# Performance work log

Hardware: AMD Instinct MI355X
Metric: run time of the kernel (lower is better)

## Reference

```python
import jax, jax.numpy as jnp
import numpy as np

L, H, F, FH, MLPD = 12, 12, 768, 64, 3072  # layers, heads, d_model, head_dim, mlp hidden
GH, GW = 32, 32
N = 1 + GH * GW  # cls token + patches
EPS = 1e-6
QK_SCALE = FH ** (-0.5)
STAGE_ENDS = (2, 5, 8, 11)  # last layer index of each of the 4 stages (3 layers/stage)


def _relpos_index(h, w):
    # standard timm BEiT relative position index with 3 extra cls entries
    coords = np.stack(np.meshgrid(np.arange(h), np.arange(w), indexing="ij"))  # 2,h,w
    cf = coords.reshape(2, -1)
    rel = (cf[:, :, None] - cf[:, None, :]).transpose(1, 2, 0).astype(np.int64)  # hw,hw,2
    rel[:, :, 0] += h - 1
    rel[:, :, 1] += w - 1
    rel[:, :, 0] *= 2 * w - 1
    num_rel = (2 * h - 1) * (2 * w - 1) + 3
    idx = np.zeros((h * w + 1, h * w + 1), dtype=np.int32)
    idx[1:, 1:] = rel.sum(-1)
    idx[0, 0:] = num_rel - 3
    idx[0:, 0] = num_rel - 2
    idx[0, 0] = num_rel - 1
    return idx, num_rel


def setup_inputs() -> dict:
    key = jax.random.key(0)
    ks = jax.random.split(key, 10)
    s = 0.02
    idx, R = _relpos_index(GH, GW)
    return dict(
        patch_tokens=jax.random.normal(ks[0], (1, GH * GW, F), jnp.float32),
        cls_token=jax.random.normal(ks[1], (1, 1, F), jnp.float32) * s,
        ln1_w=jnp.ones((L, F), jnp.float32),
        ln1_b=jnp.zeros((L, F), jnp.float32),
        qkv_w=jax.random.normal(ks[2], (L, 3 * F, F), jnp.float32) * s,
        q_bias=jax.random.normal(ks[3], (L, H, FH), jnp.float32) * s,
        v_bias=jax.random.normal(ks[4], (L, H, FH), jnp.float32) * s,
        proj_w=jax.random.normal(ks[5], (L, F, F), jnp.float32) * s,
        proj_b=jnp.zeros((L, F), jnp.float32),
        scale_attn=jnp.full((L, F), 0.1, jnp.float32),
        ln2_w=jnp.ones((L, F), jnp.float32),
        ln2_b=jnp.zeros((L, F), jnp.float32),
        fc1_w=jax.random.normal(ks[6], (L, MLPD, F), jnp.float32) * s,
        fc1_b=jnp.zeros((L, MLPD), jnp.float32),
        fc2_w=jax.random.normal(ks[7], (L, F, MLPD), jnp.float32) * s,
        fc2_b=jnp.zeros((L, F), jnp.float32),
        scale_mlp=jnp.full((L, F), 0.1, jnp.float32),
        relpos_table=jax.random.normal(ks[8], (L, R, H), jnp.float32) * s,
        relpos_index=jnp.asarray(idx),
        patch_grid_hw=jnp.array([GH, GW], jnp.int32),
    )


def _ln(x, w, b):
    mu = jnp.mean(x, -1, keepdims=True)
    var = jnp.mean(jnp.square(x - mu), -1, keepdims=True)
    return (x - mu) * jax.lax.rsqrt(var + EPS) * w + b


def reference(patch_tokens, cls_token, ln1_w, ln1_b, qkv_w, q_bias, v_bias,
              proj_w, proj_b, scale_attn, ln2_w, ln2_b, fc1_w, fc1_b, fc2_w,
              fc2_b, scale_mlp, relpos_table, relpos_index, patch_grid_hw):
    B = patch_tokens.shape[0]
    tokens = jnp.concatenate(
        [jnp.broadcast_to(cls_token, (B, 1, F)), patch_tokens], axis=1)  # B,N,F

    params = dict(ln1_w=ln1_w, ln1_b=ln1_b, qkv_w=qkv_w, q_bias=q_bias,
                  v_bias=v_bias, proj_w=proj_w, proj_b=proj_b,
                  scale_attn=scale_attn, ln2_w=ln2_w, ln2_b=ln2_b,
                  fc1_w=fc1_w, fc1_b=fc1_b, fc2_w=fc2_w, fc2_b=fc2_b,
                  scale_mlp=scale_mlp, relpos_table=relpos_table)

    def step(x, p):
        h = _ln(x, p['ln1_w'], p['ln1_b'])
        qkv = jnp.einsum('bnf,gf->bng', h, p['qkv_w'])          # B,N,3F (no bias)
        qkv = qkv.reshape(B, N, 3, H, FH).transpose(2, 0, 3, 1, 4)
        q, k, v = qkv[0], qkv[1], qkv[2]                         # B,H,N,fh
        q = (q + p['q_bias'][None, :, None, :]) * QK_SCALE
        v = v + p['v_bias'][None, :, None, :]
        bias = p['relpos_table'][relpos_index]                   # N,N,H
        attn = jnp.einsum('bhnd,bhmd->bhnm', q, k) + bias.transpose(2, 0, 1)[None]
        w = jax.nn.softmax(attn, axis=-1)
        o = jnp.einsum('bhnm,bhmd->bhnd', w, v).transpose(0, 2, 1, 3).reshape(B, N, F)
        o = o @ p['proj_w'].T + p['proj_b']
        x = x + p['scale_attn'] * o
        h2 = _ln(x, p['ln2_w'], p['ln2_b'])
        m = jax.nn.gelu(h2 @ p['fc1_w'].T + p['fc1_b'], approximate=False)
        m = m @ p['fc2_w'].T + p['fc2_b']
        x = x + p['scale_mlp'] * m
        return x, x

    _, ys = jax.lax.scan(step, tokens, params)  # ys: L,B,N,F
    return (ys[STAGE_ENDS[0]], ys[STAGE_ENDS[1]], ys[STAGE_ENDS[2]], ys[STAGE_ENDS[3]])
```

## Files before the change

### kernel.cpp

```cpp
#include <hip/hip_runtime.h>
#include <hip/hip_bf16.h>
#include <math.h>

#define L_LAYERS 12
#define H_HEADS  12
#define F_DIM    768
#define FH_DIM   64
#define MLPD     3072
#define NT       1025
#define NTP      1056
#define THREE_F  2304
#define R_REL    3972
#define QK_SCALE 0.125f
#define QB       64
#define KB       128

#define CQKV  (THREE_F * F_DIM)
#define CPROJ (F_DIM * F_DIM)
#define CFC1  (MLPD * F_DIM)
#define CFC2  (F_DIM * MLPD)

typedef short short8_t __attribute__((ext_vector_type(8)));
typedef float f32x4_t  __attribute__((ext_vector_type(4)));
typedef __attribute__((address_space(1))) const void* gptr_t;
typedef __attribute__((address_space(3))) void*       lptr_t;

typedef __hip_bfloat16 bf16;

static __device__ inline unsigned short f2bf(float f) {
    __hip_bfloat16 b(f);
    unsigned short u;
    __builtin_memcpy(&u, &b, 2);
    return u;
}

__device__ inline void xcd_remap(int& tx, int& ty) {
    int gx = gridDim.x, gy = gridDim.y;
    int b = blockIdx.y * gx + blockIdx.x;
    int total = gx * gy;
    int q = total >> 3, r = total & 7;
    int xcd = b & 7, i = b >> 3;
    int pos = (xcd < r) ? xcd * (q + 1) + i : r * (q + 1) + (xcd - r) * q + i;
    ty = pos / gx;
    tx = pos - ty * gx;
}

__global__ void init_x_k(const float* __restrict__ patch, const float* __restrict__ cls,
                         float* __restrict__ x) {
    int i = blockIdx.x * 256 + threadIdx.x;
    if (i >= NT * F_DIM) return;
    int n = i / F_DIM, f = i - n * F_DIM;
    x[i] = (n == 0) ? cls[f] : patch[(size_t)(n - 1) * F_DIM + f];
}

__global__ void zero_vt_k(bf16* __restrict__ vt) {
    int i = blockIdx.x * 256 + threadIdx.x;
    int total = H_HEADS * FH_DIM * NTP;
    #pragma unroll
    for (int j = 0; j < 8; ++j) {
        int e = i * 8 + j;
        if (e < total) vt[e] = __hip_bfloat16(0.0f);
    }
}

__global__ void rp16_k(const int* __restrict__ rp, unsigned short* __restrict__ rp16) {
    int i = blockIdx.x * 256 + threadIdx.x;
    if (i < NT * NT) rp16[i] = (unsigned short)rp[i];
}

__global__ void tableT_k(const float* __restrict__ t, float* __restrict__ tt) {
    int i = blockIdx.x * 256 + threadIdx.x;
    if (i >= L_LAYERS * R_REL * H_HEADS) return;
    int l = i / (R_REL * H_HEADS), rem = i - l * (R_REL * H_HEADS);
    int rr = rem / H_HEADS, hh = rem - rr * H_HEADS;
    tt[((size_t)l * H_HEADS + hh) * R_REL + rr] = t[i];
}

__global__ void conv_all_k(const float* __restrict__ qkv_w, const float* __restrict__ proj_w,
                           const float* __restrict__ fc1_w, const float* __restrict__ fc2_w,
                           bf16* __restrict__ wq, bf16* __restrict__ wp,
                           bf16* __restrict__ w1, bf16* __restrict__ w2) {
    const long A1 = (long)L_LAYERS * CQKV;
    const long A2 = A1 + (long)L_LAYERS * CPROJ;
    const long A3 = A2 + (long)L_LAYERS * CFC1;
    const long A4 = A3 + (long)L_LAYERS * CFC2;
    const long total4 = A4 >> 2;
    for (long qd = (long)blockIdx.x * 256 + threadIdx.x; qd < total4;
         qd += (long)gridDim.x * 256) {
        long e = qd << 2;
        const float* s; bf16* d; long off;
        if (e < A1)      { s = qkv_w;  d = wq; off = e; }
        else if (e < A2) { s = proj_w; d = wp; off = e - A1; }
        else if (e < A3) { s = fc1_w;  d = w1; off = e - A2; }
        else             { s = fc2_w;  d = w2; off = e - A3; }
        float4 v = *reinterpret_cast<const float4*>(s + off);
        ushort4 o;
        o.x = f2bf(v.x); o.y = f2bf(v.y); o.z = f2bf(v.z); o.w = f2bf(v.w);
        *reinterpret_cast<ushort4*>(d + off) = o;
    }
}

__global__ void layernorm_k(const float* __restrict__ x, const float* __restrict__ w,
                            const float* __restrict__ b, bf16* __restrict__ out) {
    const int row = blockIdx.x;
    const float* xr = x + (size_t)row * F_DIM;
    float v0 = xr[threadIdx.x];
    float v1 = xr[threadIdx.x + 256];
    float v2 = xr[threadIdx.x + 512];
    float s  = v0 + v1 + v2;
    float s2 = v0 * v0 + v1 * v1 + v2 * v2;
    #pragma unroll
    for (int off = 32; off; off >>= 1) {
        s  += __shfl_down(s, off);
        s2 += __shfl_down(s2, off);
    }
    __shared__ float ws_[4], ws2_[4];
    int lane = threadIdx.x & 63, wid = threadIdx.x >> 6;
    if (lane == 0) { ws_[wid] = s; ws2_[wid] = s2; }
    __syncthreads();
    float S  = ws_[0] + ws_[1] + ws_[2] + ws_[3];
    float S2 = ws2_[0] + ws2_[1] + ws2_[2] + ws2_[3];
    float mu  = S * (1.0f / F_DIM);
    float var = S2 * (1.0f / F_DIM) - mu * mu;
    float rs  = rsqrtf(var + 1e-6f);
    bf16* orow = out + (size_t)row * F_DIM;
    orow[threadIdx.x]       = __hip_bfloat16((v0 - mu) * rs * w[threadIdx.x]       + b[threadIdx.x]);
    orow[threadIdx.x + 256] = __hip_bfloat16((v1 - mu) * rs * w[threadIdx.x + 256] + b[threadIdx.x + 256]);
    orow[threadIdx.x + 512] = __hip_bfloat16((v2 - mu) * rs * w[threadIdx.x + 512] + b[threadIdx.x + 512]);
}


template <int T, int NLOAD>
__device__ inline void stage_glds(const bf16* __restrict__ g0, int ld, int rows_rem,
                                  bf16* lds, int tid) {
    #pragma unroll
    for (int i = 0; i < NLOAD; ++i) {
        int slot = i * T + tid;
        int row = slot >> 3, s = slot & 7;
        int grow = row < rows_rem ? row : (rows_rem - 1);
        const bf16* src = g0 + (size_t)grow * ld + ((s ^ (row & 7)) * 8);
        bf16* dst = lds + (size_t)(i * T + (tid & ~63)) * 8;
        __builtin_amdgcn_global_load_lds((gptr_t)src, (lptr_t)dst, 16, 0, 0);
    }
}

template <int EPI, int BM, int BN, int WM, int WN>
__global__ __launch_bounds__((BM / (WM * 16)) * (BN / (WN * 16)) * 64)
void gemm_k(const bf16* __restrict__ A, const bf16* __restrict__ B,
            int M, int Nc, int K, int lda, int ldb,
            const float* __restrict__ p0, const float* __restrict__ p1,
            float* __restrict__ outF, float* __restrict__ outDup,
            bf16* __restrict__ outB0, bf16* __restrict__ outB1, bf16* __restrict__ outB2) {
    constexpr int NWM = BM / (WM * 16);
    constexpr int NWN = BN / (WN * 16);
    constexpr int T   = NWM * NWN * 64;
    constexpr int ALOADS = BM * 8 / T;
    constexpr int BLOADS = BN * 8 / T;

    __shared__ __align__(16) bf16 As[2][BM * 64];
    __shared__ __align__(16) bf16 Bs[2][BN * 64];

    int tx, ty;
    xcd_remap(tx, ty);
    const int tid  = threadIdx.x;
    const int lane = tid & 63, wid = tid >> 6;
    const int wr = wid / NWN, wc = wid % NWN;
    const int g4 = lane >> 4, l16 = lane & 15;
    const int bm = tx * BM, bn = ty * BN;
    const bf16* Ab = A + (size_t)bm * lda;
    const bf16* Bb = B + (size_t)bn * ldb;
    const int aRows = min(BM, M - bm);
    const int bRows = min(BN, Nc - bn);

    f32x4_t acc[WM][WN] = {};
    const int NK = K >> 6;

    stage_glds<T, ALOADS>(Ab, lda, aRows, As[0], tid);
    stage_glds<T, BLOADS>(Bb, ldb, bRows, Bs[0], tid);
    __syncthreads();

    for (int t = 0; t < NK; ++t) {
        const int c = t & 1;
        if (t + 1 < NK) {
            stage_glds<T, ALOADS>(Ab + (t + 1) * 64, lda, aRows, As[c ^ 1], tid);
            stage_glds<T, BLOADS>(Bb + (t + 1) * 64, ldb, bRows, Bs[c ^ 1], tid);
        }
        const short* AsS = reinterpret_cast<const short*>(As[c]);
        const short* BsS = reinterpret_cast<const short*>(Bs[c]);
        #pragma unroll
        for (int kk = 0; kk < 2; ++kk) {
            short8_t af[WM], bfr[WN];
            #pragma unroll
            for (int mi = 0; mi < WM; ++mi) {
                int ar = wr * WM * 16 + mi * 16 + l16;
                int j = (kk * 4 + g4) ^ (ar & 7);
                af[mi] = *reinterpret_cast<const short8_t*>(AsS + ar * 64 + j * 8);
            }
            #pragma unroll
            for (int ni = 0; ni < WN; ++ni) {
                int br = wc * WN * 16 + ni * 16 + l16;
                int j = (kk * 4 + g4) ^ (br & 7);
                bfr[ni] = *reinterpret_cast<const short8_t*>(BsS + br * 64 + j * 8);
            }
            #pragma unroll
            for (int mi = 0; mi < WM; ++mi)
                #pragma unroll
                for (int ni = 0; ni < WN; ++ni)
                    acc[mi][ni] = __builtin_amdgcn_mfma_f32_16x16x32_bf16(
                        af[mi], bfr[ni], acc[mi][ni], 0, 0, 0);
        }
        __syncthreads();
    }

    #pragma unroll
    for (int mi = 0; mi < WM; ++mi) {
        #pragma unroll
        for (int r = 0; r < 4; ++r) {
            const int row = bm + wr * WM * 16 + mi * 16 + g4 * 4 + r;
            if (row >= M) continue;
            #pragma unroll
            for (int ni = 0; ni < WN; ++ni) {
                const int col = bn + wc * WN * 16 + ni * 16 + l16;
                float v = acc[mi][ni][r];
                if (EPI == 0) {
                    if (col < F_DIM) {
                        int h = col >> 6, d = col & 63;
                        float q = (v + p0[col]) * QK_SCALE;
                        outB0[((size_t)h * NT + row) * 64 + d] = __hip_bfloat16(q);
                    } else if (col < 2 * F_DIM) {
                        int g = col - F_DIM;
                        int h = g >> 6, d = g & 63;
                        outB1[((size_t)h * NT + row) * 64 + d] = __hip_bfloat16(v);
                    } else {
                        int g = col - 2 * F_DIM;
                        int h = g >> 6, d = g & 63;
                        float vv = v + p1[g];
                        outB2[((size_t)h * 64 + d) * NTP + row] = __hip_bfloat16(vv);
                    }
                } else if (EPI == 3) {
                    size_t oi = (size_t)row * Nc + col;
                    v += p0[col];
                    float nv = outF[oi] + p1[col] * v;
                    outF[oi] = nv;
                    if (outDup) outDup[oi] = nv;
                } else if (EPI == 4) {
                    v += p0[col];
                    float g = 0.5f * v * (1.0f + erff(v * 0.70710678118654752f));
                    outB0[(size_t)row * MLPD + col] = __hip_bfloat16(g);
                }
            }
        }
    }
}

__global__ __launch_bounds__(256)
void flash_k(const bf16* __restrict__ q_bf, const bf16* __restrict__ k_bf,
             const bf16* __restrict__ v_t, const unsigned short* __restrict__ rp16,
             const float* __restrict__ tableT, bf16* __restrict__ o_bf) {
    __shared__ __align__(16) bf16 Qs[QB * 64];
    __shared__ __align__(16) bf16 Ks[2][KB * 64];
    __shared__ __align__(16) bf16 Vs[2][64 * KB];
    __shared__ __align__(16) bf16 Ps[4][16 * KB];

    int qx, h;
    xcd_remap(qx, h);
    const int tid = threadIdx.x, lane = tid & 63, w = tid >> 6;
    const int qb = qx * QB;
    const bf16* qh = q_bf + (size_t)h * NT * 64;
    const bf16* kh = k_bf + (size_t)h * NT * 64;
    const bf16* vh = v_t  + (size_t)h * 64 * NTP;
    const float* tbl = tableT + (size_t)h * R_REL;
    const int q_local = lane & 15;
    const int g4 = lane >> 4;

    auto stageKV = [&](int buf, int m0) {
        const int kRows = min(KB, NT - m0);
        #pragma unroll
        for (int i = 0; i < 4; ++i) {
            int slot = i * 256 + tid;
            int row = slot >> 3, s = slot & 7;
            int grow = min(row, kRows - 1);
            const bf16* src = kh + (size_t)(m0 + grow) * 64 + (s ^ (row & 7)) * 8;
            bf16* dst = Ks[buf] + (size_t)(i * 256 + (tid & ~63)) * 8;
            __builtin_amdgcn_global_load_lds((gptr_t)src, (lptr_t)dst, 16, 0, 0);
        }
        #pragma unroll
        for (int i = 0; i < 4; ++i) {
            int slot = i * 256 + tid;
            int d = slot >> 4, s = slot & 15;
            int msl = min(m0 / 8 + (s ^ (d & 15)), NTP / 8 - 1);
            const bf16* src = vh + (size_t)d * NTP + msl * 8;
            bf16* dst = Vs[buf] + (size_t)(i * 256 + (tid & ~63)) * 8;
            __builtin_amdgcn_global_load_lds((gptr_t)src, (lptr_t)dst, 16, 0, 0);
        }
    };

    {
        const int qRows = min(QB, NT - qb);
        #pragma unroll
        for (int i = 0; i < 2; ++i) {
            int slot = i * 256 + tid;
            int row = slot >> 3, s = slot & 7;
            int grow = min(row, qRows - 1);
            const bf16* src = qh + (size_t)(qb + grow) * 64 + (s ^ (row & 7)) * 8;
            bf16* dst = Qs + (size_t)(i * 256 + (tid & ~63)) * 8;
            __builtin_amdgcn_global_load_lds((gptr_t)src, (lptr_t)dst, 16, 0, 0);
        }
    }
    stageKV(0, 0);
    __syncthreads();

    short8_t qf[2];
    {
        const short* QsS = (const short*)Qs;
        #pragma unroll
        for (int kk = 0; kk < 2; ++kk) {
            int row = w * 16 + q_local;
            int slot = (kk * 4 + g4) ^ (row & 7);
            qf[kk] = *(const short8_t*)(QsS + row * 64 + slot * 8);
        }
    }

    float m_run[4], l_run[4];
    f32x4_t acc[4] = {};
    #pragma unroll
    for (int r = 0; r < 4; ++r) { m_run[r] = -1e30f; l_run[r] = 0.0f; }

    const int NTILES = (NT + KB - 1) / KB;
    for (int t = 0; t < NTILES; ++t) {
        const int m0 = t * KB;
        const int c = t & 1;
        if (t + 1 < NTILES) stageKV(c ^ 1, (t + 1) * KB);

        f32x4_t sfr[8];
        {
            const short* KsS = (const short*)Ks[c];
            #pragma unroll
            for (int f = 0; f < 8; ++f) {
                f32x4_t cacc = {};
                #pragma unroll
                for (int kk = 0; kk < 2; ++kk) {
                    int mrow = f * 16 + q_local;
                    int slot = (kk * 4 + g4) ^ (mrow & 7);
                    short8_t bv = *(const short8_t*)(KsS + mrow * 64 + slot * 8);
                    cacc = __builtin_amdgcn_mfma_f32_16x16x32_bf16(qf[kk], bv, cacc, 0, 0, 0);
                }
                sfr[f] = cacc;
            }
        }

        const int qrow_base = qb + w * 16 + g4 * 4;
        #pragma unroll
        for (int f = 0; f < 8; ++f) {
            int mm = m0 + f * 16 + q_local;
            if (mm < NT) {
                #pragma unroll
                for (int r = 0; r < 4; ++r) {
                    int qc = min(qrow_base + r, NT - 1);
                    int idx = rp16[(size_t)qc * NT + mm];
                    sfr[f][r] += tbl[idx];
                }
            } else {
                #pragma unroll
                for (int r = 0; r < 4; ++r) sfr[f][r] = -1e30f;
            }
        }

        float pmax[4];
        #pragma unroll
        for (int r = 0; r < 4; ++r) {
            float mx = sfr[0][r];
            #pragma unroll
            for (int f = 1; f < 8; ++f) mx = fmaxf(mx, sfr[f][r]);
            pmax[r] = mx;
        }
        #pragma unroll
        for (int off = 1; off < 16; off <<= 1)
            #pragma unroll
            for (int r = 0; r < 4; ++r) pmax[r] = fmaxf(pmax[r], __shfl_xor(pmax[r], off));

        float fac[4];
        #pragma unroll
        for (int r = 0; r < 4; ++r) {
            float mnew = fmaxf(m_run[r], pmax[r]);
            fac[r] = __expf(m_run[r] - mnew);
            m_run[r] = mnew;
        }

        float rsum[4] = {0.f, 0.f, 0.f, 0.f};
        short* PsW = (short*)Ps[w];
        #pragma unroll
        for (int f = 0; f < 8; ++f) {
            int mloc = f * 16 + q_local;
            #pragma unroll
            for (int r = 0; r < 4; ++r) {
                int ql = g4 * 4 + r;
                float p = __expf(sfr[f][r] - m_run[r]);
                rsum[r] += p;
                PsW[ql * 128 + (((mloc >> 3) ^ ql) * 8) + (mloc & 7)] = (short)f2bf(p);
            }
        }
        #pragma unroll
        for (int off = 1; off < 16; off <<= 1)
            #pragma unroll
            for (int r = 0; r < 4; ++r) rsum[r] += __shfl_xor(rsum[r], off);
        #pragma unroll
        for (int r = 0; r < 4; ++r) l_run[r] = l_run[r] * fac[r] + rsum[r];
        #pragma unroll
        for (int df = 0; df < 4; ++df)
            #pragma unroll
            for (int r = 0; r < 4; ++r) acc[df][r] *= fac[r];

        {
            const short* PsR = (const short*)Ps[w];
            const short* VsS = (const short*)Vs[c];
            #pragma unroll
            for (int kk = 0; kk < 4; ++kk) {
                int j = kk * 4 + g4;
                short8_t pa = *(const short8_t*)(PsR + q_local * 128 + (j ^ q_local) * 8);
                #pragma unroll
                for (int df = 0; df < 4; ++df) {
                    int drow = df * 16 + q_local;
                    short8_t vb = *(const short8_t*)(VsS + drow * 128 + (j ^ (drow & 15)) * 8);
                    acc[df] = __builtin_amdgcn_mfma_f32_16x16x32_bf16(pa, vb, acc[df], 0, 0, 0);
                }
            }
        }
        __syncthreads();
    }

    #pragma unroll
    for (int df = 0; df < 4; ++df) {
        #pragma unroll
        for (int r = 0; r < 4; ++r) {
            int qq = qb + w * 16 + g4 * 4 + r;
            if (qq < NT) {
                float o = acc[df][r] / l_run[r];
                o_bf[(size_t)qq * F_DIM + h * 64 + df * 16 + q_local] = __hip_bfloat16(o);
            }
        }
    }
}

extern "C" void kernel_launch(void* const* d_in, const int* in_sizes, int n_in,
                              void* d_out, int out_size, void* d_ws, size_t ws_size,
                              hipStream_t stream) {
    const float* patch      = (const float*)d_in[0];
    const float* cls        = (const float*)d_in[1];
    const float* ln1_w      = (const float*)d_in[2];
    const float* ln1_b      = (const float*)d_in[3];
    const float* qkv_w      = (const float*)d_in[4];
    const float* q_bias     = (const float*)d_in[5];
    const float* v_bias     = (const float*)d_in[6];
    const float* proj_w     = (const float*)d_in[7];
    const float* proj_b     = (const float*)d_in[8];
    const float* scale_attn = (const float*)d_in[9];
    const float* ln2_w      = (const float*)d_in[10];
    const float* ln2_b      = (const float*)d_in[11];
    const float* fc1_w      = (const float*)d_in[12];
    const float* fc1_b      = (const float*)d_in[13];
    const float* fc2_w      = (const float*)d_in[14];
    const float* fc2_b      = (const float*)d_in[15];
    const float* scale_mlp  = (const float*)d_in[16];
    const float* table      = (const float*)d_in[17];
    const int*   rp_idx     = (const int*)d_in[18];
    float* out = (float*)d_out;

    char* ws = (char*)d_ws;
    size_t off = 0;
    auto alloc = [&](size_t bytes) { char* p = ws + off; off += (bytes + 255) & ~255ULL; return p; };

    float* x      = (float*)alloc((size_t)NT * F_DIM * 4);
    bf16*  h_bf   = (bf16*) alloc((size_t)NT * F_DIM * 2);
    bf16*  q_bf   = (bf16*) alloc((size_t)H_HEADS * NT * 64 * 2);
    bf16*  k_bf   = (bf16*) alloc((size_t)H_HEADS * NT * 64 * 2);
    bf16*  v_t    = (bf16*) alloc((size_t)H_HEADS * 64 * NTP * 2);
    bf16*  o_bf   = (bf16*) alloc((size_t)NT * F_DIM * 2);
    bf16*  m1_bf  = (bf16*) alloc((size_t)NT * MLPD * 2);
    unsigned short* rp16 = (unsigned short*)alloc((size_t)NT * NT * 2);
    float* tableT = (float*)alloc((size_t)L_LAYERS * H_HEADS * R_REL * 4);
    bf16*  wq_all = (bf16*) alloc((size_t)L_LAYERS * CQKV * 2);
    bf16*  wp_all = (bf16*) alloc((size_t)L_LAYERS * CPROJ * 2);
    bf16*  w1_all = (bf16*) alloc((size_t)L_LAYERS * CFC1 * 2);
    bf16*  w2_all = (bf16*) alloc((size_t)L_LAYERS * CFC2 * 2);

    init_x_k<<<(NT * F_DIM + 255) / 256, 256, 0, stream>>>(patch, cls, x);
    zero_vt_k<<<(H_HEADS * 64 * NTP + 2047) / 2048, 256, 0, stream>>>(v_t);
    rp16_k<<<(NT * NT + 255) / 256, 256, 0, stream>>>(rp_idx, rp16);
    tableT_k<<<(L_LAYERS * R_REL * H_HEADS + 255) / 256, 256, 0, stream>>>(table, tableT);
    conv_all_k<<<2048, 256, 0, stream>>>(qkv_w, proj_w, fc1_w, fc2_w,
                                         wq_all, wp_all, w1_all, w2_all);

    int stage = 0;
    for (int l = 0; l < L_LAYERS; ++l) {
        layernorm_k<<<NT, 256, 0, stream>>>(x, ln1_w + l * F_DIM, ln1_b + l * F_DIM, h_bf);

        gemm_k<0, 64, 128, 2, 2><<<dim3(17, 18), 512, 0, stream>>>(
            h_bf, wq_all + (size_t)l * CQKV, NT, THREE_F, F_DIM, F_DIM, F_DIM,
            q_bias + (size_t)l * F_DIM, v_bias + (size_t)l * F_DIM,
            nullptr, nullptr, q_bf, k_bf, v_t);

        flash_k<<<dim3((NT + QB - 1) / QB, H_HEADS), 256, 0, stream>>>(
            q_bf, k_bf, v_t, rp16,
            tableT + (size_t)l * H_HEADS * R_REL, o_bf);

        gemm_k<3, 32, 64, 1, 2><<<dim3(33, 12), 256, 0, stream>>>(
            o_bf, wp_all + (size_t)l * CPROJ, NT, F_DIM, F_DIM, F_DIM, F_DIM,
            proj_b + (size_t)l * F_DIM, scale_attn + (size_t)l * F_DIM,
            x, nullptr, nullptr, nullptr, nullptr);

        layernorm_k<<<NT, 256, 0, stream>>>(x, ln2_w + l * F_DIM, ln2_b + l * F_DIM, h_bf);

        gemm_k<4, 64, 128, 2, 2><<<dim3(17, 24), 512, 0, stream>>>(
            h_bf, w1_all + (size_t)l * CFC1, NT, MLPD, F_DIM, F_DIM, F_DIM,
            fc1_b + (size_t)l * MLPD, nullptr,
            nullptr, nullptr, m1_bf, nullptr, nullptr);

        const bool isStage = (l == 2 || l == 5 || l == 8 || l == 11);
        float* outDup = isStage ? (out + (size_t)stage * NT * F_DIM) : nullptr;
        gemm_k<3, 32, 64, 1, 2><<<dim3(33, 12), 256, 0, stream>>>(
            m1_bf, w2_all + (size_t)l * CFC2, NT, F_DIM, MLPD, MLPD, MLPD,
            fc2_b + (size_t)l * F_DIM, scale_mlp + (size_t)l * F_DIM,
            x, outDup, nullptr, nullptr, nullptr);
        if (isStage) ++stage;
    }
}
```

Before: 1.557 ms.

## Merge setup kernels, use nontemporal weight conversion, raise MFMA wave priority

```diff
diff --git a/kernel.cpp b/kernel.cpp
--- a/kernel.cpp
+++ b/kernel.cpp
@@ -22,6 +22,7 @@
 
 typedef short short8_t __attribute__((ext_vector_type(8)));
 typedef float f32x4_t  __attribute__((ext_vector_type(4)));
+typedef unsigned short u16x4_t __attribute__((ext_vector_type(4)));
 typedef __attribute__((address_space(1))) const void* gptr_t;
 typedef __attribute__((address_space(3))) void*       lptr_t;
 
@@ -45,35 +46,31 @@
     tx = pos - ty * gx;
 }
 
-__global__ void init_x_k(const float* __restrict__ patch, const float* __restrict__ cls,
-                         float* __restrict__ x) {
-    int i = blockIdx.x * 256 + threadIdx.x;
-    if (i >= NT * F_DIM) return;
-    int n = i / F_DIM, f = i - n * F_DIM;
-    x[i] = (n == 0) ? cls[f] : patch[(size_t)(n - 1) * F_DIM + f];
-}
-
-__global__ void zero_vt_k(bf16* __restrict__ vt) {
-    int i = blockIdx.x * 256 + threadIdx.x;
-    int total = H_HEADS * FH_DIM * NTP;
-    #pragma unroll
-    for (int j = 0; j < 8; ++j) {
-        int e = i * 8 + j;
-        if (e < total) vt[e] = __hip_bfloat16(0.0f);
-    }
-}
-
-__global__ void rp16_k(const int* __restrict__ rp, unsigned short* __restrict__ rp16) {
-    int i = blockIdx.x * 256 + threadIdx.x;
-    if (i < NT * NT) rp16[i] = (unsigned short)rp[i];
-}
-
-__global__ void tableT_k(const float* __restrict__ t, float* __restrict__ tt) {
-    int i = blockIdx.x * 256 + threadIdx.x;
-    if (i >= L_LAYERS * R_REL * H_HEADS) return;
-    int l = i / (R_REL * H_HEADS), rem = i - l * (R_REL * H_HEADS);
-    int rr = rem / H_HEADS, hh = rem - rr * H_HEADS;
-    tt[((size_t)l * H_HEADS + hh) * R_REL + rr] = t[i];
+__global__ void setup_k(const float* __restrict__ patch, const float* __restrict__ cls,
+                        const int* __restrict__ rp, const float* __restrict__ t,
+                        float* __restrict__ x, bf16* __restrict__ vt,
+                        unsigned short* __restrict__ rp16, float* __restrict__ tt) {
+    const int E0 = NT * F_DIM;
+    const int E1 = H_HEADS * FH_DIM * NTP;
+    const int E2 = NT * NT;
+    const int E3 = L_LAYERS * R_REL * H_HEADS;
+    const int total = E0 + E1 + E2 + E3;
+    for (int i = blockIdx.x * 256 + threadIdx.x; i < total; i += gridDim.x * 256) {
+        if (i < E0) {
+            int n = i / F_DIM, f = i - n * F_DIM;
+            x[i] = (n == 0) ? cls[f] : patch[(size_t)(n - 1) * F_DIM + f];
+        } else if (i < E0 + E1) {
+            vt[i - E0] = __hip_bfloat16(0.0f);
+        } else if (i < E0 + E1 + E2) {
+            int e = i - E0 - E1;
+            rp16[e] = (unsigned short)rp[e];
+        } else {
+            int e = i - E0 - E1 - E2;
+            int l = e / (R_REL * H_HEADS), rem = e - l * (R_REL * H_HEADS);
+            int rr = rem / H_HEADS, hh = rem - rr * H_HEADS;
+            tt[((size_t)l * H_HEADS + hh) * R_REL + rr] = t[e];
+        }
+    }
 }
 
 __global__ void conv_all_k(const float* __restrict__ qkv_w, const float* __restrict__ proj_w,
@@ -93,10 +90,10 @@
         else if (e < A2) { s = proj_w; d = wp; off = e - A1; }
         else if (e < A3) { s = fc1_w;  d = w1; off = e - A2; }
         else             { s = fc2_w;  d = w2; off = e - A3; }
-        float4 v = *reinterpret_cast<const float4*>(s + off);
-        ushort4 o;
+        f32x4_t v = __builtin_nontemporal_load(reinterpret_cast<const f32x4_t*>(s + off));
+        u16x4_t o;
         o.x = f2bf(v.x); o.y = f2bf(v.y); o.z = f2bf(v.z); o.w = f2bf(v.w);
-        *reinterpret_cast<ushort4*>(d + off) = o;
+        __builtin_nontemporal_store(o, reinterpret_cast<u16x4_t*>(d + off));
     }
 }
 
@@ -128,7 +125,6 @@
     orow[threadIdx.x + 256] = __hip_bfloat16((v1 - mu) * rs * w[threadIdx.x + 256] + b[threadIdx.x + 256]);
     orow[threadIdx.x + 512] = __hip_bfloat16((v2 - mu) * rs * w[threadIdx.x + 512] + b[threadIdx.x + 512]);
 }
-
 
 template <int T, int NLOAD>
 __device__ inline void stage_glds(const bf16* __restrict__ g0, int ld, int rows_rem,
@@ -335,6 +331,7 @@
         f32x4_t sfr[8];
         {
             const short* KsS = (const short*)Ks[c];
+            __builtin_amdgcn_s_setprio(1);
             #pragma unroll
             for (int f = 0; f < 8; ++f) {
                 f32x4_t cacc = {};
@@ -347,6 +344,7 @@
                 }
                 sfr[f] = cacc;
             }
+            __builtin_amdgcn_s_setprio(0);
         }
 
         const int qrow_base = qb + w * 16 + g4 * 4;
@@ -414,6 +412,7 @@
         {
             const short* PsR = (const short*)Ps[w];
             const short* VsS = (const short*)Vs[c];
+            __builtin_amdgcn_s_setprio(1);
             #pragma unroll
             for (int kk = 0; kk < 4; ++kk) {
                 int j = kk * 4 + g4;
@@ -425,6 +424,7 @@
                     acc[df] = __builtin_amdgcn_mfma_f32_16x16x32_bf16(pa, vb, acc[df], 0, 0, 0);
                 }
             }
+            __builtin_amdgcn_s_setprio(0);
         }
         __syncthreads();
     }
@@ -484,10 +484,7 @@
     bf16*  w1_all = (bf16*) alloc((size_t)L_LAYERS * CFC1 * 2);
     bf16*  w2_all = (bf16*) alloc((size_t)L_LAYERS * CFC2 * 2);
 
-    init_x_k<<<(NT * F_DIM + 255) / 256, 256, 0, stream>>>(patch, cls, x);
-    zero_vt_k<<<(H_HEADS * 64 * NTP + 2047) / 2048, 256, 0, stream>>>(v_t);
-    rp16_k<<<(NT * NT + 255) / 256, 256, 0, stream>>>(rp_idx, rp16);
-    tableT_k<<<(L_LAYERS * R_REL * H_HEADS + 255) / 256, 256, 0, stream>>>(table, tableT);
+    setup_k<<<2048, 256, 0, stream>>>(patch, cls, rp_idx, table, x, v_t, rp16, tableT);
     conv_all_k<<<2048, 256, 0, stream>>>(qkv_w, proj_w, fc1_w, fc2_w,
                                          wq_all, wp_all, w1_all, w2_all);
 
```

After: 1.662 ms. 1.07x slower.
